# Optimization experiments

Hardware: AMD Instinct MI355X
Metric: run time of the kernel (lower is better)

The kernel has to match this reference:

```python
import jax, jax.numpy as jnp
import numpy as np

B = 500_000      # batch rows
F = 100          # fixed by x.view(-1, 100)
NT = 10          # number of tails (clusters)
C = 10           # cluster size (features per tail)
H = 7            # hidden = ceil(0.75 * C)


def setup_inputs() -> dict:
    key = jax.random.key(0)
    ks = jax.random.split(key, 7)
    x = jax.random.normal(ks[0], (B, F), dtype=jnp.float32)
    Wt = jax.random.normal(ks[1], (NT, H, C), dtype=jnp.float32) * 0.1
    hbias_t = jax.random.normal(ks[2], (NT, H), dtype=jnp.float32) * 0.1
    vbias_t = jax.random.normal(ks[3], (NT, C), dtype=jnp.float32) * 0.1
    Wh = jax.random.normal(ks[4], (H, NT), dtype=jnp.float32) * 0.1
    hbias_h = jax.random.normal(ks[5], (H,), dtype=jnp.float32) * 0.1
    vbias_h = jax.random.normal(ks[6], (NT,), dtype=jnp.float32) * 0.1
    clusters = jnp.arange(F, dtype=jnp.int32).reshape(NT, C)
    return {"x": x, "Wt": Wt, "hbias_t": hbias_t, "vbias_t": vbias_t,
            "Wh": Wh, "hbias_h": hbias_h, "vbias_h": vbias_h,
            "clusters": clusters}


def reference(x, Wt, hbias_t, vbias_t, Wh, hbias_h, vbias_h, clusters):
    x = x.reshape(-1, F)
    # fused gather: [B, NT, C]
    xc = x[:, clusters]
    # tail encoders: z = xc @ We.T + hbias  (We = Wt[t], shape [H, C])
    z = jnp.einsum('btc,thc->bth', xc, Wt) + hbias_t[None]          # [B, NT, H]
    # tail decoders (tied weights W.T): out = z @ We + vbias
    out = jnp.einsum('bth,thc->btc', z, Wt) + vbias_t[None]          # [B, NT, C]
    # per-sample, per-tail RMSE then log
    rmse = jnp.sqrt(jnp.mean((out - xc) ** 2, axis=-1))              # [B, NT]
    tails = jnp.log(rmse)                                            # [B, NT]
    # head autoencoder over tail scores
    zh = tails @ Wh.T + hbias_h                                      # [B, H]
    head_out = zh @ Wh + vbias_h                                     # [B, NT]
    return head_out, tails
```

## Files before the change

### kernel.cpp

```cpp
#include <hip/hip_runtime.h>


typedef float v2f __attribute__((ext_vector_type(2)));

constexpr int F  = 100;
constexpr int NT = 10;
constexpr int C  = 10;
constexpr int H  = 7;
constexpr int BLOCK = 512;
constexpr int RPB   = 64;
constexpr int CHUNK_BYTES = RPB * F * 4;
constexpr int NOPS = CHUNK_BYTES / 1024;

__device__ __forceinline__ int tail_col(int t) {
    return (t < 8) ? 10 * t : (t == 8 ? 61 : 71);
}

__device__ __forceinline__ void stage_issue(const float* __restrict__ x,
                                            long long chunk, float* lds,
                                            int wave, int lane, int tot_ops)
{
    const char* g0 = (const char*)x + chunk * (long long)CHUNK_BYTES + lane * 16;
    char* l0 = (char*)lds;
    for (int op = wave; op < tot_ops; op += 8) {
        __builtin_amdgcn_global_load_lds(
            (const __attribute__((address_space(1))) void*)(g0 + op * 1024),
            (__attribute__((address_space(3))) void*)(l0 + op * 1024),
            16, 0, 0);
    }
}

__device__ __forceinline__ void do_tile(
    int t,
    float* __restrict__ xrow,
    const float* __restrict__ Wt,
    const float* __restrict__ hbt,
    const float* __restrict__ vbt)
{
    const int cb = t * 10;
    const v2f* __restrict__ xr2 = (const v2f*)(xrow + cb);
    v2f xc[5];
    #pragma unroll
    for (int c2 = 0; c2 < 5; ++c2) xc[c2] = xr2[c2];

    v2f out[5];
    #pragma unroll
    for (int c2 = 0; c2 < 5; ++c2) {
        out[c2].x = vbt[t * C + 2 * c2];
        out[c2].y = vbt[t * C + 2 * c2 + 1];
    }
    #pragma unroll
    for (int h = 0; h < H; ++h) {
        v2f w[5];
        #pragma unroll
        for (int c2 = 0; c2 < 5; ++c2) {
            w[c2].x = Wt[(t * H + h) * C + 2 * c2];
            w[c2].y = Wt[(t * H + h) * C + 2 * c2 + 1];
        }
        v2f za; za.x = hbt[t * H + h]; za.y = 0.f;
        #pragma unroll
        for (int c2 = 0; c2 < 5; ++c2)
            za = __builtin_elementwise_fma(xc[c2], w[c2], za);
        const float z = za.x + za.y;
        v2f zz; zz.x = z; zz.y = z;
        #pragma unroll
        for (int c2 = 0; c2 < 5; ++c2)
            out[c2] = __builtin_elementwise_fma(zz, w[c2], out[c2]);
    }
    v2f a2; a2.x = 0.f; a2.y = 0.f;
    #pragma unroll
    for (int c2 = 0; c2 < 5; ++c2) {
        const v2f d = out[c2] - xc[c2];
        a2 = __builtin_elementwise_fma(d, d, a2);
    }
    const float acc = a2.x + a2.y;
    xrow[tail_col(t)] = 0.5f * __logf(acc * 0.1f);
}

__global__ __launch_bounds__(BLOCK, 6) void kitnet_main(
    const float* __restrict__ x,
    const float* __restrict__ Wt,
    const float* __restrict__ hbt,
    const float* __restrict__ vbt,
    const float* __restrict__ Wh,
    const float* __restrict__ hbh,
    const float* __restrict__ vbh,
    float* __restrict__ head_out,
    float* __restrict__ tails_out,
    int B)
{
    __shared__ float xs[2][RPB * F];

    const int tid  = threadIdx.x;
    const int lane = tid & 63;
    const int wave = __builtin_amdgcn_readfirstlane(tid >> 6);

    const long long nchunks = ((long long)B + RPB - 1) / RPB;
    long long chunk = blockIdx.x;
    const int G = gridDim.x;
    if (chunk >= nchunks) return;

    {
        const long long rows0 = ((long long)B - chunk * RPB >= RPB)
                                    ? RPB : ((long long)B - chunk * RPB);
        const int tot0 = (int)((rows0 * F * 4 + 1023) / 1024);
        stage_issue(x, chunk, xs[0], wave, lane, tot0);
    }

    int cur = 0;
    for (; chunk < nchunks; chunk += G, cur ^= 1) {
        const long long nxt = chunk + G;
        const bool has_next  = (nxt < nchunks);
        const bool next_full = has_next && (nxt * RPB + RPB <= (long long)B);

        if (has_next) {
            int tot = NOPS;
            if (!next_full) {
                const long long rows = (long long)B - nxt * RPB;
                tot = (int)((rows * F * 4 + 1023) / 1024);
            }
            stage_issue(x, nxt, xs[cur ^ 1], wave, lane, tot);
        }

        if (next_full) {
            if (wave == 0) asm volatile("s_waitcnt vmcnt(4)" ::: "memory");
            else           asm volatile("s_waitcnt vmcnt(3)" ::: "memory");
        } else {
            asm volatile("s_waitcnt vmcnt(0)" ::: "memory");
        }
        asm volatile("s_barrier" ::: "memory");

        const long long rem = (long long)B - chunk * RPB;
        const int nrows = (rem >= RPB) ? RPB : (int)rem;
        float* xrow = &xs[cur][lane * F];
        if (lane < nrows) {
            do_tile(wave, xrow, Wt, hbt, vbt);
            if (wave >= 6) do_tile(wave + 2, xrow, Wt, hbt, vbt);
        }

        asm volatile("s_waitcnt lgkmcnt(0)" ::: "memory");
        __builtin_amdgcn_sched_barrier(0);
        asm volatile("s_barrier" ::: "memory");

        const int ntask = nrows * 5;
        if (tid < ntask) {
            const int row = tid / 5;
            const int c0  = (tid - row * 5) * 2;
            const float* __restrict__ trow = &xs[cur][row * F];
            float tl[NT];
            #pragma unroll
            for (int t = 0; t < NT; ++t) tl[t] = trow[tail_col(t)];
            float zh[H];
            #pragma unroll
            for (int h = 0; h < H; ++h) {
                float s = hbh[h];
                #pragma unroll
                for (int t = 0; t < NT; ++t) s = fmaf(tl[t], Wh[h * NT + t], s);
                zh[h] = s;
            }
            float h0 = vbh[c0], h1 = vbh[c0 + 1];
            #pragma unroll
            for (int h = 0; h < H; ++h) {
                h0 = fmaf(zh[h], Wh[h * NT + c0],     h0);
                h1 = fmaf(zh[h], Wh[h * NT + c0 + 1], h1);
            }
            const long long o = (chunk * RPB + row) * NT + c0;
            v2f hv; hv.x = h0; hv.y = h1;
            v2f tv; tv.x = trow[tail_col(c0)]; tv.y = trow[tail_col(c0 + 1)];
            *(v2f*)(head_out  + o) = hv;
            *(v2f*)(tails_out + o) = tv;
        }

        asm volatile("s_barrier" ::: "memory");
    }
}

extern "C" void kernel_launch(void* const* d_in, const int* in_sizes, int n_in,
                              void* d_out, int out_size, void* d_ws, size_t ws_size,
                              hipStream_t stream) {
    const float* x   = (const float*)d_in[0];
    const float* Wt  = (const float*)d_in[1];
    const float* hbt = (const float*)d_in[2];
    const float* vbt = (const float*)d_in[3];
    const float* Wh  = (const float*)d_in[4];
    const float* hbh = (const float*)d_in[5];
    const float* vbh = (const float*)d_in[6];
    const int B = in_sizes[0] / F;
    float* head  = (float*)d_out;
    float* tails = head + (size_t)B * NT;
    const long long nchunks = ((long long)B + RPB - 1) / RPB;
    const int grid = (int)((nchunks < 768) ? nchunks : 768);
    kitnet_main<<<grid, BLOCK, 0, stream>>>(x, Wt, hbt, vbt, Wh, hbh, vbh,
                                            head, tails, B);
}
```

Baseline: 299.6 us.

## Triple-buffer LDS staging to prefetch two chunks ahead

Switches the LDS staging of x from double to triple buffering, so loads for chunk k+2G are issued while chunk k is computed, and waits for chunk k+G only at the end of each iteration. It also clamps the tail-chunk addresses to the end of x and lowers occupancy (launch bounds 4, grid 512) to fit the larger LDS footprint. The aim is to hide more HBM latency in this bandwidth-bound kernel. In exchange it uses fewer resident blocks and relies on hand-tuned vmcnt counts that must match the per-wave load counts.

```diff
diff --git a/kernel.cpp b/kernel.cpp
--- a/kernel.cpp
+++ b/kernel.cpp
@@ -9,24 +9,31 @@
 constexpr int H  = 7;
 constexpr int BLOCK = 512;
 constexpr int RPB   = 64;
-constexpr int CHUNK_BYTES = RPB * F * 4;
-constexpr int NOPS = CHUNK_BYTES / 1024;
+constexpr long long CHUNK_BYTES = (long long)RPB * F * 4;
 
 __device__ __forceinline__ int tail_col(int t) {
     return (t < 8) ? 10 * t : (t == 8 ? 61 : 71);
 }
 
-__device__ __forceinline__ void stage_issue(const float* __restrict__ x,
-                                            long long chunk, float* lds,
-                                            int wave, int lane, int tot_ops)
+__device__ __forceinline__ void stage_issue(const char* g0,
+                                            char* l0, int wave, int tot_ops,
+                                            const char* gmax, bool clampit)
 {
-    const char* g0 = (const char*)x + chunk * (long long)CHUNK_BYTES + lane * 16;
-    char* l0 = (char*)lds;
-    for (int op = wave; op < tot_ops; op += 8) {
-        __builtin_amdgcn_global_load_lds(
-            (const __attribute__((address_space(1))) void*)(g0 + op * 1024),
-            (__attribute__((address_space(3))) void*)(l0 + op * 1024),
-            16, 0, 0);
+    if (!clampit) {
+        for (int op = wave; op < tot_ops; op += 8)
+            __builtin_amdgcn_global_load_lds(
+                (const __attribute__((address_space(1))) void*)(g0 + op * 1024),
+                (__attribute__((address_space(3))) void*)(l0 + op * 1024),
+                16, 0, 0);
+    } else {
+        for (int op = wave; op < tot_ops; op += 8) {
+            const char* ga = g0 + op * 1024;
+            if (ga > gmax) ga = gmax;
+            __builtin_amdgcn_global_load_lds(
+                (const __attribute__((address_space(1))) void*)ga,
+                (__attribute__((address_space(3))) void*)(l0 + op * 1024),
+                16, 0, 0);
+        }
     }
 }
 
@@ -77,7 +84,7 @@
     xrow[tail_col(t)] = 0.5f * __logf(acc * 0.1f);
 }
 
-__global__ __launch_bounds__(BLOCK, 6) void kitnet_main(
+__global__ __launch_bounds__(BLOCK, 4) void kitnet_main(
     const float* __restrict__ x,
     const float* __restrict__ Wt,
     const float* __restrict__ hbt,
@@ -89,55 +96,65 @@
     float* __restrict__ tails_out,
     int B)
 {
-    __shared__ float xs[2][RPB * F];
+    __shared__ float xs[3][RPB * F];
 
     const int tid  = threadIdx.x;
     const int lane = tid & 63;
     const int wave = __builtin_amdgcn_readfirstlane(tid >> 6);
 
     const long long nchunks = ((long long)B + RPB - 1) / RPB;
-    long long chunk = blockIdx.x;
+    const long long xbytes  = (long long)B * F * 4;
+    const char* xb   = (const char*)x;
+    const char* gmax = xb + xbytes - 16;
     const int G = gridDim.x;
-    if (chunk >= nchunks) return;
+    long long k = blockIdx.x;
+    if (k >= nchunks) return;
 
     {
-        const long long rows0 = ((long long)B - chunk * RPB >= RPB)
-                                    ? RPB : ((long long)B - chunk * RPB);
-        const int tot0 = (int)((rows0 * F * 4 + 1023) / 1024);
-        stage_issue(x, chunk, xs[0], wave, lane, tot0);
-    }
-
-    int cur = 0;
-    for (; chunk < nchunks; chunk += G, cur ^= 1) {
-        const long long nxt = chunk + G;
-        const bool has_next  = (nxt < nchunks);
-        const bool next_full = has_next && (nxt * RPB + RPB <= (long long)B);
-
-        if (has_next) {
-            int tot = NOPS;
-            if (!next_full) {
-                const long long rows = (long long)B - nxt * RPB;
-                tot = (int)((rows * F * 4 + 1023) / 1024);
-            }
-            stage_issue(x, nxt, xs[cur ^ 1], wave, lane, tot);
-        }
-
-        if (next_full) {
+        const long long b0 = xbytes - k * CHUNK_BYTES;
+        const bool f0 = b0 >= CHUNK_BYTES;
+        const int  t0 = f0 ? 25 : (int)((b0 + 1023) >> 10);
+        stage_issue(xb + k * CHUNK_BYTES + lane * 16, (char*)xs[0], wave, t0,
+                    gmax, !f0);
+        const long long k1 = k + G;
+        bool f1 = false;
+        if (k1 < nchunks) {
+            const long long b1 = xbytes - k1 * CHUNK_BYTES;
+            f1 = b1 >= CHUNK_BYTES;
+            const int t1 = f1 ? 25 : (int)((b1 + 1023) >> 10);
+            stage_issue(xb + k1 * CHUNK_BYTES + lane * 16, (char*)xs[1], wave,
+                        t1, gmax, !f1);
+        }
+        if (f1) {
             if (wave == 0) asm volatile("s_waitcnt vmcnt(4)" ::: "memory");
             else           asm volatile("s_waitcnt vmcnt(3)" ::: "memory");
         } else {
             asm volatile("s_waitcnt vmcnt(0)" ::: "memory");
         }
+        __builtin_amdgcn_sched_barrier(0);
         asm volatile("s_barrier" ::: "memory");
-
-        const long long rem = (long long)B - chunk * RPB;
+    }
+
+    int cur = 0;
+    for (; k < nchunks; k += G, cur = (cur == 2 ? 0 : cur + 1)) {
+        const long long k2 = k + 2LL * G;
+        bool f2 = false;
+        if (k2 < nchunks) {
+            const long long b2 = xbytes - k2 * CHUNK_BYTES;
+            f2 = b2 >= CHUNK_BYTES;
+            const int t2 = f2 ? 25 : (int)((b2 + 1023) >> 10);
+            const int slot = (cur + 2 >= 3) ? cur - 1 : cur + 2;
+            stage_issue(xb + k2 * CHUNK_BYTES + lane * 16, (char*)xs[slot],
+                        wave, t2, gmax, !f2);
+        }
+
+        const long long rem = (long long)B - k * RPB;
         const int nrows = (rem >= RPB) ? RPB : (int)rem;
         float* xrow = &xs[cur][lane * F];
         if (lane < nrows) {
             do_tile(wave, xrow, Wt, hbt, vbt);
             if (wave >= 6) do_tile(wave + 2, xrow, Wt, hbt, vbt);
         }
-
         asm volatile("s_waitcnt lgkmcnt(0)" ::: "memory");
         __builtin_amdgcn_sched_barrier(0);
         asm volatile("s_barrier" ::: "memory");
@@ -164,14 +181,24 @@
                 h0 = fmaf(zh[h], Wh[h * NT + c0],     h0);
                 h1 = fmaf(zh[h], Wh[h * NT + c0 + 1], h1);
             }
-            const long long o = (chunk * RPB + row) * NT + c0;
+            const long long o = (k * RPB + row) * NT + c0;
             v2f hv; hv.x = h0; hv.y = h1;
             v2f tv; tv.x = trow[tail_col(c0)]; tv.y = trow[tail_col(c0 + 1)];
             *(v2f*)(head_out  + o) = hv;
             *(v2f*)(tails_out + o) = tv;
         }
 
-        asm volatile("s_barrier" ::: "memory");
+        if (k + G < nchunks) {
+            if (f2) {
+                if (wave == 0)      asm volatile("s_waitcnt vmcnt(6)" ::: "memory");
+                else if (wave < 5)  asm volatile("s_waitcnt vmcnt(5)" ::: "memory");
+                else                asm volatile("s_waitcnt vmcnt(3)" ::: "memory");
+            } else {
+                asm volatile("s_waitcnt vmcnt(0)" ::: "memory");
+            }
+            __builtin_amdgcn_sched_barrier(0);
+            asm volatile("s_barrier" ::: "memory");
+        }
     }
 }
 
@@ -189,7 +216,7 @@
     float* head  = (float*)d_out;
     float* tails = head + (size_t)B * NT;
     const long long nchunks = ((long long)B + RPB - 1) / RPB;
-    const int grid = (int)((nchunks < 768) ? nchunks : 768);
+    const int grid = (int)((nchunks < 512) ? nchunks : 512);
     kitnet_main<<<grid, BLOCK, 0, stream>>>(x, Wt, hbt, vbt, Wh, hbh, vbh,
                                             head, tails, B);
 }
```

Result: slower. 306.9 us (+2.5%).
